# Kernel optimization log

Measured on AMD Instinct MI355X. Metric: run time of the kernel, lower is better.

## Reference

```python
import jax, jax.numpy as jnp
import numpy as np

BATCH, SEQ, D_MODEL = 8, 2048, 512
HEADS, BUCKET, N_HASHES = 8, 4, 4
D_HEAD = D_MODEL // HEADS
N_BUCKETS = SEQ // BUCKET
SELF_ATTN_VAL = -5e4  # TOKEN_SELF_ATTN_VALUE in reformer-pytorch


def setup_inputs() -> dict:
    key = jax.random.key(0)
    ks = jax.random.split(key, 8)
    scale = 1.0 / np.sqrt(D_MODEL).astype(np.float32)
    q = jax.random.normal(ks[0], (BATCH, SEQ, D_MODEL), jnp.float32)
    k = jax.random.normal(ks[1], (BATCH, SEQ, D_MODEL), jnp.float32)
    v = jax.random.normal(ks[2], (BATCH, SEQ, D_MODEL), jnp.float32)
    Wqk = jax.random.normal(ks[3], (D_MODEL, D_MODEL), jnp.float32) * scale
    Wv = jax.random.normal(ks[4], (D_MODEL, D_MODEL), jnp.float32) * scale
    Wout = jax.random.normal(ks[5], (D_MODEL, D_MODEL), jnp.float32) * scale
    b_out = jnp.zeros((D_MODEL,), jnp.float32)
    rotations = jax.random.normal(ks[6], (D_HEAD, N_HASHES, N_BUCKETS // 2), jnp.float32)
    return {"queries": q, "keys": k, "values": v, "Wqk": Wqk, "Wv": Wv,
            "Wout": Wout, "b_out": b_out, "rotations": rotations}


def _look_one_back(x):
    # concat each chunk with the previous chunk (wrap-around), along within-chunk axis
    return jnp.concatenate([x, jnp.roll(x, 1, axis=1)], axis=2)


def _lsh_attend(qk, v, rotations, bucket_size, n_hashes):
    # qk, v: (bm, t, d); shared-QK LSH attention (reformer-pytorch defaults)
    bm, t, d = qk.shape
    n_buckets = t // bucket_size
    # --- hash ---
    rotated = jnp.einsum('btf,fhi->bhti', qk, rotations)          # (bm, nh, t, nb/2)
    rotated = jnp.concatenate([rotated, -rotated], axis=-1)       # (bm, nh, t, nb)
    buckets = jnp.argmax(rotated, axis=-1)                        # (bm, nh, t)
    offsets = (jnp.arange(n_hashes) * n_buckets)[None, :, None]
    buckets = (buckets + offsets).reshape(bm, n_hashes * t)
    # --- sort tokens by (bucket, position) ---
    ticker = jnp.arange(n_hashes * t)
    buckets_and_t = t * buckets + (ticker % t)[None, :]           # unique values
    sticker = jnp.argsort(buckets_and_t, axis=-1)                 # (bm, nh*t)
    undo_sort = jnp.argsort(sticker, axis=-1)
    st = sticker % t
    sqk = jnp.take_along_axis(qk, st[:, :, None], axis=1)         # (bm, nh*t, d)
    sv = jnp.take_along_axis(v, st[:, :, None], axis=1)
    # --- chunk ---
    n_chunks = n_hashes * n_buckets
    bq_t = st.reshape(bm, n_chunks, bucket_size)
    bqk = sqk.reshape(bm, n_chunks, bucket_size, d)
    bv = sv.reshape(bm, n_chunks, bucket_size, d)
    bq = bqk
    norm = jnp.maximum(jnp.linalg.norm(bqk, axis=-1, keepdims=True), 1e-12)
    bk = bqk / norm                                               # F.normalize (shared QK)
    bk = _look_one_back(bk)
    bv = _look_one_back(bv)
    bkv_t = jnp.concatenate([bq_t, jnp.roll(bq_t, 1, axis=1)], axis=2)
    # --- attend within chunks ---
    dots = jnp.einsum('bnie,bnje->bnij', bq, bk) * (d ** -0.5)    # (bm, nc, bs, 2bs)
    self_mask = bq_t[:, :, :, None] == bkv_t[:, :, None, :]
    dots = jnp.where(self_mask, SELF_ATTN_VAL, dots)
    dots_lse = jax.nn.logsumexp(dots, axis=-1, keepdims=True)
    probs = jnp.exp(dots - dots_lse)
    bo = jnp.einsum('bnij,bnje->bnie', probs, bv)
    so = bo.reshape(bm, -1, d)
    slogits = dots_lse.reshape(bm, -1)
    # --- unsort and combine hash rounds ---
    o = jnp.take_along_axis(so, undo_sort[:, :, None], axis=1)
    logits = jnp.take_along_axis(slogits, undo_sort, axis=1)
    o = o.reshape(bm, n_hashes, t, d)
    logits = logits.reshape(bm, n_hashes, t, 1)
    w = jnp.exp(logits - jax.nn.logsumexp(logits, axis=1, keepdims=True))
    return jnp.sum(o * w, axis=1)                                 # (bm, t, d)


def reference(queries, keys, values, Wqk, Wv, Wout, b_out, rotations):
    # keys/values are unused by the original module (self-attention on queries)
    B, N, C = queries.shape
    H, d = HEADS, C // HEADS
    qk = jnp.einsum('bnc,cd->bnd', queries, Wqk)
    v = jnp.einsum('bnc,cd->bnd', queries, Wv)
    qk = qk.reshape(B, N, H, d).transpose(0, 2, 1, 3).reshape(B * H, N, d)
    v = v.reshape(B, N, H, d).transpose(0, 2, 1, 3).reshape(B * H, N, d)
    o = _lsh_attend(qk, v, rotations, BUCKET, N_HASHES)
    o = o.reshape(B, H, N, d).transpose(0, 2, 1, 3).reshape(B, N, C)
    return jnp.einsum('bnc,cd->bnd', o, Wout) + b_out
```

## Files before the change

kernel.cpp:

```cpp
#include <hip/hip_runtime.h>
#include <math.h>

#define SELF_VAL (-5e4f)

typedef __attribute__((ext_vector_type(8))) short bf16x8;
typedef __attribute__((ext_vector_type(4))) float f32x4;

__device__ __forceinline__ unsigned short f2bf(float x) {
    unsigned b = __float_as_uint(x);
    b += 0x7FFFu + ((b >> 16) & 1u);
    return (unsigned short)(b >> 16);
}
__device__ __forceinline__ float bf2f(unsigned short h) {
    return __uint_as_float(((unsigned)h) << 16);
}

__global__ __launch_bounds__(256) void k_rotT(const float* __restrict__ rot,
                                              float* __restrict__ rotT2)
{
    int idx = blockIdx.x * 256 + threadIdx.x;
    int h = idx >> 14, k = (idx >> 8) & 63, col = idx & 255;
    rotT2[idx] = rot[k * 1024 + h * 256 + col];
}

__global__ __launch_bounds__(256) void k_woutT(const float* __restrict__ Wout,
                                               unsigned short* __restrict__ WoutT16)
{
    int idx = blockIdx.x * 256 + threadIdx.x;
    int n = idx >> 9, k = idx & 511;
    WoutT16[idx] = f2bf(Wout[(size_t)k * 512 + n]);
}

__global__ __launch_bounds__(256) void k_wvT(const float* __restrict__ Wv,
                                             unsigned short* __restrict__ WvT16)
{
    int idx = blockIdx.x * 256 + threadIdx.x;
    int n = idx >> 9, k = idx & 511;
    WvT16[idx] = f2bf(Wv[(size_t)k * 512 + n]);
}

__global__ __launch_bounds__(256) void k_q16(const float* __restrict__ Q,
                                             unsigned short* __restrict__ Q16)
{
    int idx = blockIdx.x * 256 + threadIdx.x;
    const float* src = Q + (size_t)idx * 8;
    float4 v0 = *(const float4*)src;
    float4 v1 = *(const float4*)(src + 4);
    union { unsigned short s[8]; uint4 v; } ob;
    ob.s[0]=f2bf(v0.x); ob.s[1]=f2bf(v0.y); ob.s[2]=f2bf(v0.z); ob.s[3]=f2bf(v0.w);
    ob.s[4]=f2bf(v1.x); ob.s[5]=f2bf(v1.y); ob.s[6]=f2bf(v1.z); ob.s[7]=f2bf(v1.w);
    *(uint4*)(Q16 + (size_t)idx * 8) = ob.v;
}

__global__ __launch_bounds__(256) void k_gemm_qk(
    const float* __restrict__ Q, const float* __restrict__ Wqk,
    float* __restrict__ qk, float* __restrict__ rnorm)
{
    __shared__ float As[16][132];
    __shared__ float Bs[16][132];
    const int bx = blockIdx.x;
    const int mt = bx >> 2, nt = bx & 3;
    const int m0 = mt * 128, n0 = nt * 128;
    const int tid = threadIdx.x;
    const int ty = tid >> 4, tx = tid & 15;
    const float* Bsrc = Wqk + n0;
    const int ar0 = tid >> 2, acq = (tid & 3) * 4;
    const int ar1 = 64 + (tid >> 2);
    const int bk0 = tid >> 5, bnq = (tid & 31) * 4;
    const int bk1 = 8 + (tid >> 5);
    const float* Aptr0 = Q + (size_t)(m0 + ar0) * 512 + acq;
    const float* Aptr1 = Q + (size_t)(m0 + ar1) * 512 + acq;
    const float* Bptr0 = Bsrc + (size_t)bk0 * 512 + bnq;
    const float* Bptr1 = Bsrc + (size_t)bk1 * 512 + bnq;
    float acc[8][8] = {};
    float4 a0 = *(const float4*)(Aptr0);
    float4 a1 = *(const float4*)(Aptr1);
    float4 b0 = *(const float4*)(Bptr0);
    float4 b1 = *(const float4*)(Bptr1);
    for (int k0 = 0; k0 < 512; k0 += 16) {
        As[acq+0][ar0]=a0.x; As[acq+1][ar0]=a0.y; As[acq+2][ar0]=a0.z; As[acq+3][ar0]=a0.w;
        As[acq+0][ar1]=a1.x; As[acq+1][ar1]=a1.y; As[acq+2][ar1]=a1.z; As[acq+3][ar1]=a1.w;
        *(float4*)&Bs[bk0][bnq] = b0;
        *(float4*)&Bs[bk1][bnq] = b1;
        __syncthreads();
        if (k0 + 16 < 512) {
            a0 = *(const float4*)(Aptr0 + k0 + 16);
            a1 = *(const float4*)(Aptr1 + k0 + 16);
            b0 = *(const float4*)(Bptr0 + (size_t)(k0 + 16) * 512);
            b1 = *(const float4*)(Bptr1 + (size_t)(k0 + 16) * 512);
        }
        #pragma unroll
        for (int kk = 0; kk < 16; kk++) {
            float a_[8], b_[8];
            *(float4*)&a_[0] = *(float4*)&As[kk][ty*4];
            *(float4*)&a_[4] = *(float4*)&As[kk][64 + ty*4];
            *(float4*)&b_[0] = *(float4*)&Bs[kk][tx*4];
            *(float4*)&b_[4] = *(float4*)&Bs[kk][64 + tx*4];
            #pragma unroll
            for (int i = 0; i < 8; i++)
                #pragma unroll
                for (int j = 0; j < 8; j++)
                    acc[i][j] += a_[i] * b_[j];
        }
        __syncthreads();
    }
    #pragma unroll
    for (int ig = 0; ig < 2; ig++) {
        #pragma unroll
        for (int i = 0; i < 4; i++) {
            int row = m0 + ig*64 + ty*4 + i;
            int b = row >> 11, t = row & 2047;
            #pragma unroll
            for (int jg = 0; jg < 2; jg++) {
                int n = n0 + jg*64 + tx*4;
                float4 r4 = make_float4(acc[ig*4+i][jg*4+0], acc[ig*4+i][jg*4+1],
                                        acc[ig*4+i][jg*4+2], acc[ig*4+i][jg*4+3]);
                *(float4*)(qk + ((size_t)((b*8 + (n>>6))*2048 + t))*64 + (n&63)) = r4;
            }
        }
    }
    #pragma unroll
    for (int jg = 0; jg < 2; jg++) {
        int h = (n0 + jg*64) >> 6;
        #pragma unroll
        for (int ig = 0; ig < 2; ig++) {
            #pragma unroll
            for (int i = 0; i < 4; i++) {
                float s = acc[ig*4+i][jg*4+0]*acc[ig*4+i][jg*4+0]
                        + acc[ig*4+i][jg*4+1]*acc[ig*4+i][jg*4+1]
                        + acc[ig*4+i][jg*4+2]*acc[ig*4+i][jg*4+2]
                        + acc[ig*4+i][jg*4+3]*acc[ig*4+i][jg*4+3];
                s += __shfl_xor(s, 1);
                s += __shfl_xor(s, 2);
                s += __shfl_xor(s, 4);
                s += __shfl_xor(s, 8);
                if (tx == 0) {
                    int row = m0 + ig*64 + ty*4 + i;
                    int b = row >> 11, t = row & 2047;
                    rnorm[((size_t)(b*8 + h))*2048 + t] = 1.0f / fmaxf(sqrtf(s), 1e-12f);
                }
            }
        }
    }
}

__global__ __launch_bounds__(256) void k_gemm_v(
    const unsigned short* __restrict__ Q16, const unsigned short* __restrict__ WvT16,
    float* __restrict__ vv)
{
    __shared__ unsigned short Asl[64*72];
    __shared__ unsigned short Bsl[64*72];
    const int bx = blockIdx.x;
    const int mt = bx >> 3, nt = bx & 7;
    const int m0 = mt*64, n0 = nt*64;
    const int tid = threadIdx.x;
    const int wid = tid >> 6, lane = tid & 63;
    const int wm = wid >> 1, wn = wid & 1;
    const int l15 = lane & 15, l4 = lane >> 4;
    const int srow = tid >> 2, skb = (tid & 3) * 16;
    f32x4 acc[2][2] = {};
    for (int k0 = 0; k0 < 512; k0 += 64) {
        {
            const unsigned short* asrc = Q16 + (size_t)(m0 + srow)*512 + k0 + skb;
            *(uint4*)&Asl[srow*72 + skb]     = *(const uint4*)asrc;
            *(uint4*)&Asl[srow*72 + skb + 8] = *(const uint4*)(asrc + 8);
            const unsigned short* bsrc = WvT16 + (size_t)(n0 + srow)*512 + k0 + skb;
            *(uint4*)&Bsl[srow*72 + skb]     = *(const uint4*)bsrc;
            *(uint4*)&Bsl[srow*72 + skb + 8] = *(const uint4*)(bsrc + 8);
        }
        __syncthreads();
        #pragma unroll
        for (int kq = 0; kq < 2; kq++) {
            int kb = kq*32 + l4*8;
            bf16x8 a0 = *(bf16x8*)&Asl[(wm*32 +      l15)*72 + kb];
            bf16x8 a1 = *(bf16x8*)&Asl[(wm*32 + 16 + l15)*72 + kb];
            bf16x8 b0 = *(bf16x8*)&Bsl[(wn*32 +      l15)*72 + kb];
            bf16x8 b1 = *(bf16x8*)&Bsl[(wn*32 + 16 + l15)*72 + kb];
            acc[0][0] = __builtin_amdgcn_mfma_f32_16x16x32_bf16(a0, b0, acc[0][0], 0, 0, 0);
            acc[0][1] = __builtin_amdgcn_mfma_f32_16x16x32_bf16(a0, b1, acc[0][1], 0, 0, 0);
            acc[1][0] = __builtin_amdgcn_mfma_f32_16x16x32_bf16(a1, b0, acc[1][0], 0, 0, 0);
            acc[1][1] = __builtin_amdgcn_mfma_f32_16x16x32_bf16(a1, b1, acc[1][1], 0, 0, 0);
        }
        __syncthreads();
    }
    #pragma unroll
    for (int sm = 0; sm < 2; sm++) {
        #pragma unroll
        for (int sn = 0; sn < 2; sn++) {
            int col = n0 + wn*32 + sn*16 + l15;
            int h = col >> 6, d = col & 63;
            #pragma unroll
            for (int r = 0; r < 4; r++) {
                int row = m0 + wm*32 + sm*16 + l4*4 + r;
                int b = row >> 11, t = row & 2047;
                vv[((size_t)((b*8 + h)*2048 + t))*64 + d] = acc[sm][sn][r];
            }
        }
    }
}

__global__ __launch_bounds__(256) void k_hash(const float* __restrict__ qk,
    const float* __restrict__ rotT2, unsigned* __restrict__ buckets)
{
    __shared__ float As[64*128];
    const int bx = blockIdx.x;
    const int bm = bx >> 4;
    const int row0 = (bx & 15) << 7;
    const int tid = threadIdx.x;
    const int ty = tid >> 4, tx = tid & 15;
    {
        const int r = tid >> 1;
        const int kb = (tid & 1) * 8;
        const float* src = qk + ((size_t)(bm*2048 + row0 + r))*64;
        #pragma unroll
        for (int c = 0; c < 8; c++) {
            float4 a4 = *(const float4*)(src + (size_t)(kb + c)*4);
            int k = (kb + c)*4;
            As[(k+0)*128 + r] = a4.x;
            As[(k+1)*128 + r] = a4.y;
            As[(k+2)*128 + r] = a4.z;
            As[(k+3)*128 + r] = a4.w;
        }
    }
    __syncthreads();
    #pragma unroll 1
    for (int h = 0; h < 4; h++) {
        float bv[8]; unsigned bi[8];
        #pragma unroll
        for (int i = 0; i < 8; i++) { bv[i] = -3.402823466e38f; bi[i] = 0u; }
        #pragma unroll 1
        for (int ch = 0; ch < 4; ch++) {
            const float* bsrc = rotT2 + (size_t)h*16384 + ch*64 + tx*4;
            float acc[8][4] = {};
            #pragma unroll 16
            for (int kk = 0; kk < 64; kk++) {
                float4 b4 = *(const float4*)(bsrc + (size_t)kk*256);
                float a_[8];
                *(float4*)&a_[0] = *(float4*)&As[kk*128 + ty*4];
                *(float4*)&a_[4] = *(float4*)&As[kk*128 + 64 + ty*4];
                float b_[4] = {b4.x, b4.y, b4.z, b4.w};
                #pragma unroll
                for (int i = 0; i < 8; i++)
                    #pragma unroll
                    for (int j = 0; j < 4; j++)
                        acc[i][j] += a_[i] * b_[j];
            }
            #pragma unroll
            for (int j = 0; j < 4; j++) {
                unsigned c0 = (unsigned)(ch*64 + tx*4 + j);
                unsigned nc0 = 256u + c0;
                #pragma unroll
                for (int i = 0; i < 8; i++) {
                    float v = acc[i][j];
                    if (v > bv[i] || (v == bv[i] && c0 < bi[i])) { bv[i] = v; bi[i] = c0; }
                    float nv = -v;
                    if (nv > bv[i] || (nv == bv[i] && nc0 < bi[i])) { bv[i] = nv; bi[i] = nc0; }
                }
            }
        }
        #pragma unroll
        for (int i = 0; i < 8; i++) {
            #pragma unroll
            for (int d = 1; d < 16; d <<= 1) {
                float ov = __shfl_xor(bv[i], d);
                unsigned oi = (unsigned)__shfl_xor((int)bi[i], d);
                if (ov > bv[i] || (ov == bv[i] && oi < bi[i])) { bv[i] = ov; bi[i] = oi; }
            }
        }
        if (tx == 0) {
            #pragma unroll
            for (int i = 0; i < 8; i++) {
                int r = (i < 4) ? (ty*4 + i) : (64 + ty*4 + (i - 4));
                buckets[((size_t)(bm*4 + h))*2048 + row0 + r] = bi[i];
            }
        }
    }
}

__global__ __launch_bounds__(256) void k_sort(const unsigned* __restrict__ buckets,
                                              unsigned* __restrict__ st)
{
    __shared__ unsigned whist[4][512];
    __shared__ unsigned baseb[512];
    const int seg = blockIdx.x;
    const unsigned* bk = buckets + (size_t)seg * 2048;
    unsigned* out = st + (size_t)seg * 2048;
    const int tid = threadIdx.x, w = tid >> 6, lane = tid & 63;
    for (int b = tid; b < 2048; b += 256) ((unsigned*)whist)[b] = 0u;
    __syncthreads();
    unsigned myb[8];
    #pragma unroll
    for (int r = 0; r < 8; r++) {
        int pos = w*512 + r*64 + lane;
        myb[r] = bk[pos];
        atomicAdd(&whist[w][myb[r]], 1u);
    }
    __syncthreads();
    for (int b = tid; b < 512; b += 256) {
        unsigned p = 0;
        #pragma unroll
        for (int ww = 0; ww < 4; ww++) { unsigned t = whist[ww][b]; whist[ww][b] = p; p += t; }
        baseb[b] = p;
    }
    __syncthreads();
    if (tid == 0) {
        unsigned run = 0;
        for (int b = 0; b < 512; b++) { unsigned t = baseb[b]; baseb[b] = run; run += t; }
    }
    __syncthreads();
    for (int b = tid; b < 512; b += 256) {
        unsigned bb = baseb[b];
        #pragma unroll
        for (int ww = 0; ww < 4; ww++) whist[ww][b] += bb;
    }
    __syncthreads();
    for (int r = 0; r < 8; r++) {
        unsigned b = myb[r];
        int pos = w*512 + r*64 + lane;
        unsigned base = whist[w][b];
        unsigned rank = 0;
        for (int j = 0; j < 64; j++) {
            unsigned bj = __shfl(b, j);
            rank += (j < lane && bj == b) ? 1u : 0u;
        }
        out[base + rank] = (unsigned)pos;
        atomicAdd(&whist[w][b], 1u);
    }
}

__global__ __launch_bounds__(256) void k_attn(const float* __restrict__ qk,
    const float* __restrict__ vv, const float* __restrict__ rnorm,
    const unsigned* __restrict__ st, unsigned short* __restrict__ oh16,
    float* __restrict__ logits)
{
    __shared__ float qs[68][68];
    __shared__ float vs[68][68];
    __shared__ unsigned P[68];
    __shared__ float rn[68];
    const int sid = blockIdx.x;
    const int stripi = sid & 31;
    const int seg = sid >> 5;
    const int bm = seg >> 2, h = seg & 3;
    const int G0 = (h*512 + stripi*16) * 4;
    const int tid = threadIdx.x;
    for (int j = tid; j < 68; j += 256) {
        int G = (G0 - 4 + j) & 8191;
        int hg = G >> 11, sg = G & 2047;
        unsigned tok = st[((size_t)(bm*4 + hg))*2048 + sg];
        P[j] = tok;
        rn[j] = rnorm[bm*2048 + (int)tok];
    }
    __syncthreads();
    for (int e = tid; e < 68*16; e += 256) {
        int j = e >> 4, fq = e & 15;
        unsigned tok = P[j];
        size_t base = ((size_t)(bm*2048 + (int)tok))*64 + fq*4;
        *(float4*)&qs[j][fq*4] = *(const float4*)(qk + base);
        *(float4*)&vs[j][fq*4] = *(const float4*)(vv + base);
    }
    __syncthreads();
    const int w = tid >> 6, lane = tid & 63;
    const int half = lane >> 5, qi = (lane >> 3) & 3, jj = lane & 7;
    const int fb = lane & 7;
    for (int cp = 0; cp < 2; cp++) {
        int c = w*4 + cp*2 + half;
        int jq = 4 + c*4 + qi;
        int jk = c*4 + jj;
        float dot = 0.f;
        #pragma unroll
        for (int fq = 0; fq < 16; fq++) {
            float4 q4 = *(float4*)&qs[jq][fq*4];
            float4 k4 = *(float4*)&qs[jk][fq*4];
            dot += q4.x*k4.x + q4.y*k4.y + q4.z*k4.z + q4.w*k4.w;
        }
        dot *= 0.125f * rn[jk];
        if (P[jq] == P[jk]) dot = SELF_VAL;
        float m = dot;
        m = fmaxf(m, __shfl_xor(m, 1));
        m = fmaxf(m, __shfl_xor(m, 2));
        m = fmaxf(m, __shfl_xor(m, 4));
        float ex = expf(dot - m);
        float s = ex;
        s += __shfl_xor(s, 1); s += __shfl_xor(s, 2); s += __shfl_xor(s, 4);
        float lse = m + logf(s);
        float p = expf(dot - lse);
        unsigned tq = P[jq];
        if (jj == 0) logits[((size_t)(bm*4 + h))*2048 + tq] = lse;
        float a0=0,a1=0,a2=0,a3=0,a4a=0,a5=0,a6=0,a7=0;
        #pragma unroll
        for (int j2 = 0; j2 < 8; j2++) {
            float pj = __shfl(p, (lane & 0x38) | j2);
            float4 va = *(float4*)&vs[c*4 + j2][fb*8];
            float4 vb = *(float4*)&vs[c*4 + j2][fb*8 + 4];
            a0 += pj*va.x; a1 += pj*va.y; a2 += pj*va.z; a3 += pj*va.w;
            a4a += pj*vb.x; a5 += pj*vb.y; a6 += pj*vb.z; a7 += pj*vb.w;
        }
        union { unsigned short s[8]; uint4 v; } ob;
        ob.s[0]=f2bf(a0); ob.s[1]=f2bf(a1); ob.s[2]=f2bf(a2); ob.s[3]=f2bf(a3);
        ob.s[4]=f2bf(a4a); ob.s[5]=f2bf(a5); ob.s[6]=f2bf(a6); ob.s[7]=f2bf(a7);
        *(uint4*)(oh16 + ((size_t)((bm*4 + h)*2048 + (int)tq))*64 + fb*8) = ob.v;
    }
}

__global__ __launch_bounds__(256) void k_combine(const unsigned short* __restrict__ oh16,
    const float* __restrict__ logits, unsigned short* __restrict__ comb16)
{
    int w = threadIdx.x >> 6, lane = threadIdx.x & 63;
    int row = blockIdx.x * 4 + w;
    int bm = row >> 11, t = row & 2047;
    int b = bm >> 3, head = bm & 7;
    float l0 = logits[((size_t)(bm*4 + 0))*2048 + t];
    float l1 = logits[((size_t)(bm*4 + 1))*2048 + t];
    float l2 = logits[((size_t)(bm*4 + 2))*2048 + t];
    float l3 = logits[((size_t)(bm*4 + 3))*2048 + t];
    float m = fmaxf(fmaxf(l0, l1), fmaxf(l2, l3));
    float e0 = expf(l0 - m), e1 = expf(l1 - m), e2 = expf(l2 - m), e3 = expf(l3 - m);
    float inv = 1.0f / (e0 + e1 + e2 + e3);
    float o = 0.f;
    o += (e0*inv) * bf2f(oh16[((size_t)((bm*4+0)*2048 + t))*64 + lane]);
    o += (e1*inv) * bf2f(oh16[((size_t)((bm*4+1)*2048 + t))*64 + lane]);
    o += (e2*inv) * bf2f(oh16[((size_t)((bm*4+2)*2048 + t))*64 + lane]);
    o += (e3*inv) * bf2f(oh16[((size_t)((bm*4+3)*2048 + t))*64 + lane]);
    comb16[((size_t)(b*2048 + t))*512 + head*64 + lane] = f2bf(o);
}

__global__ __launch_bounds__(256) void k_gemm_out(
    const unsigned short* __restrict__ comb16, const unsigned short* __restrict__ WoutT16,
    const float* __restrict__ bias, float* __restrict__ out)
{
    __shared__ unsigned short Asl[64*72];
    __shared__ unsigned short Bsl[64*72];
    const int bx = blockIdx.x;
    const int mt = bx >> 3, nt = bx & 7;
    const int m0 = mt*64, n0 = nt*64;
    const int tid = threadIdx.x;
    const int wid = tid >> 6, lane = tid & 63;
    const int wm = wid >> 1, wn = wid & 1;
    const int l15 = lane & 15, l4 = lane >> 4;
    const int srow = tid >> 2, skb = (tid & 3) * 16;
    f32x4 acc[2][2] = {};
    for (int k0 = 0; k0 < 512; k0 += 64) {
        {
            const unsigned short* asrc = comb16 + (size_t)(m0 + srow)*512 + k0 + skb;
            *(uint4*)&Asl[srow*72 + skb]     = *(const uint4*)asrc;
            *(uint4*)&Asl[srow*72 + skb + 8] = *(const uint4*)(asrc + 8);
            const unsigned short* bsrc = WoutT16 + (size_t)(n0 + srow)*512 + k0 + skb;
            *(uint4*)&Bsl[srow*72 + skb]     = *(const uint4*)bsrc;
            *(uint4*)&Bsl[srow*72 + skb + 8] = *(const uint4*)(bsrc + 8);
        }
        __syncthreads();
        #pragma unroll
        for (int kq = 0; kq < 2; kq++) {
            int kb = kq*32 + l4*8;
            bf16x8 a0 = *(bf16x8*)&Asl[(wm*32 +      l15)*72 + kb];
            bf16x8 a1 = *(bf16x8*)&Asl[(wm*32 + 16 + l15)*72 + kb];
            bf16x8 b0 = *(bf16x8*)&Bsl[(wn*32 +      l15)*72 + kb];
            bf16x8 b1 = *(bf16x8*)&Bsl[(wn*32 + 16 + l15)*72 + kb];
            acc[0][0] = __builtin_amdgcn_mfma_f32_16x16x32_bf16(a0, b0, acc[0][0], 0, 0, 0);
            acc[0][1] = __builtin_amdgcn_mfma_f32_16x16x32_bf16(a0, b1, acc[0][1], 0, 0, 0);
            acc[1][0] = __builtin_amdgcn_mfma_f32_16x16x32_bf16(a1, b0, acc[1][0], 0, 0, 0);
            acc[1][1] = __builtin_amdgcn_mfma_f32_16x16x32_bf16(a1, b1, acc[1][1], 0, 0, 0);
        }
        __syncthreads();
    }
    #pragma unroll
    for (int sm = 0; sm < 2; sm++) {
        #pragma unroll
        for (int sn = 0; sn < 2; sn++) {
            int col = n0 + wn*32 + sn*16 + l15;
            float bb = bias[col];
            #pragma unroll
            for (int r = 0; r < 4; r++) {
                int row = m0 + wm*32 + sm*16 + l4*4 + r;
                out[(size_t)row*512 + col] = acc[sm][sn][r] + bb;
            }
        }
    }
}

extern "C" void kernel_launch(void* const* d_in, const int* in_sizes, int n_in,
                              void* d_out, int out_size, void* d_ws, size_t ws_size,
                              hipStream_t stream)
{
    const float* Q    = (const float*)d_in[0];
    const float* Wqk  = (const float*)d_in[3];
    const float* Wv   = (const float*)d_in[4];
    const float* Wout = (const float*)d_in[5];
    const float* bout = (const float*)d_in[6];
    const float* rot  = (const float*)d_in[7];
    float* ws = (float*)d_ws;
    float* qk     = ws;
    float* vv     = ws + 8388608;
    unsigned short* oh16 = (unsigned short*)(ws + 16777216);
    unsigned short* WoutT16 = (unsigned short*)(ws + 33554432);
    unsigned short* Q16     = (unsigned short*)(ws + 33685504);
    unsigned short* WvT16   = (unsigned short*)(ws + 37879808);
    unsigned short* comb16  = (unsigned short*)(ws + 50331648);
    float* rnorm  = ws + 58720256;
    float* logits = ws + 58851328;
    unsigned* buckets = (unsigned*)(ws + 59375616);
    unsigned* st      = (unsigned*)(ws + 59899904);
    float* rotT2  = ws + 60424192;
    float* out = (float*)d_out;

    k_rotT    <<<dim3(256),  dim3(256), 0, stream>>>(rot, rotT2);
    k_woutT   <<<dim3(1024), dim3(256), 0, stream>>>(Wout, WoutT16);
    k_wvT     <<<dim3(1024), dim3(256), 0, stream>>>(Wv, WvT16);
    k_q16     <<<dim3(4096), dim3(256), 0, stream>>>(Q, Q16);
    k_gemm_qk <<<dim3(512),  dim3(256), 0, stream>>>(Q, Wqk, qk, rnorm);
    k_gemm_v  <<<dim3(2048), dim3(256), 0, stream>>>(Q16, WvT16, vv);
    k_hash    <<<dim3(1024), dim3(256), 0, stream>>>(qk, rotT2, buckets);
    k_sort    <<<dim3(256),  dim3(256), 0, stream>>>(buckets, st);
    k_attn    <<<dim3(8192), dim3(256), 0, stream>>>(qk, vv, rnorm, st, oh16, logits);
    k_combine <<<dim3(32768),dim3(256), 0, stream>>>(oh16, logits, comb16);
    k_gemm_out<<<dim3(2048), dim3(256), 0, stream>>>(comb16, WoutT16, bout, out);
}
```

Measured before the change: 556.6 us.

## Compute LSH hash projections with split-bf16 MFMA and fp32 fallback near ties

The hash kernel's fp32 FMA projection is replaced by MFMA bf16 matrix ops. Operands are split into hi/lo bf16 parts (three products) to approximate fp32 precision. The kernel tracks the top-two scores per row, and rows whose gap falls below a threshold are recomputed exactly in fp32 so argmax ties still resolve like the reference. In exchange, the QK GEMM epilogue writes extra hi/lo buffers, a new rotation-split kernel is added, and the fallback path runs serialized block reductions.

```diff
diff --git a/kernel.cpp b/kernel.cpp
--- a/kernel.cpp
+++ b/kernel.cpp
@@ -2,6 +2,7 @@
 #include <math.h>
 
 #define SELF_VAL (-5e4f)
+#define GAP_THR 0.004f
 
 typedef __attribute__((ext_vector_type(8))) short bf16x8;
 typedef __attribute__((ext_vector_type(4))) float f32x4;
@@ -14,6 +15,9 @@
 __device__ __forceinline__ float bf2f(unsigned short h) {
     return __uint_as_float(((unsigned)h) << 16);
 }
+__device__ __forceinline__ unsigned pk2(unsigned short a, unsigned short b) {
+    return (unsigned)a | ((unsigned)b << 16);
+}
 
 __global__ __launch_bounds__(256) void k_rotT(const float* __restrict__ rot,
                                               float* __restrict__ rotT2)
@@ -21,6 +25,18 @@
     int idx = blockIdx.x * 256 + threadIdx.x;
     int h = idx >> 14, k = (idx >> 8) & 63, col = idx & 255;
     rotT2[idx] = rot[k * 1024 + h * 256 + col];
+}
+
+__global__ __launch_bounds__(256) void k_rotsplit(const float* __restrict__ rot,
+    unsigned short* __restrict__ rotT3hi, unsigned short* __restrict__ rotT3lo)
+{
+    int idx = blockIdx.x * 256 + threadIdx.x;
+    int cg = idx >> 6, k = idx & 63;
+    float v = rot[k * 1024 + cg];
+    unsigned short hi = f2bf(v);
+    unsigned short lo = f2bf(v - bf2f(hi));
+    rotT3hi[idx] = hi;
+    rotT3lo[idx] = lo;
 }
 
 __global__ __launch_bounds__(256) void k_woutT(const float* __restrict__ Wout,
@@ -54,7 +70,8 @@
 
 __global__ __launch_bounds__(256) void k_gemm_qk(
     const float* __restrict__ Q, const float* __restrict__ Wqk,
-    float* __restrict__ qk, float* __restrict__ rnorm)
+    float* __restrict__ qk, float* __restrict__ rnorm,
+    unsigned short* __restrict__ qk16hi, unsigned short* __restrict__ qk16lo)
 {
     __shared__ float As[16][132];
     __shared__ float Bs[16][132];
@@ -115,7 +132,15 @@
                 int n = n0 + jg*64 + tx*4;
                 float4 r4 = make_float4(acc[ig*4+i][jg*4+0], acc[ig*4+i][jg*4+1],
                                         acc[ig*4+i][jg*4+2], acc[ig*4+i][jg*4+3]);
-                *(float4*)(qk + ((size_t)((b*8 + (n>>6))*2048 + t))*64 + (n&63)) = r4;
+                size_t base = ((size_t)((b*8 + (n>>6))*2048 + t))*64 + (n&63);
+                *(float4*)(qk + base) = r4;
+                unsigned short h0 = f2bf(r4.x), h1 = f2bf(r4.y), h2 = f2bf(r4.z), h3 = f2bf(r4.w);
+                unsigned short l0 = f2bf(r4.x - bf2f(h0)), l1 = f2bf(r4.y - bf2f(h1));
+                unsigned short l2 = f2bf(r4.z - bf2f(h2)), l3 = f2bf(r4.w - bf2f(h3));
+                uint2 hw = make_uint2(pk2(h0,h1), pk2(h2,h3));
+                uint2 lw = make_uint2(pk2(l0,l1), pk2(l2,l3));
+                *(uint2*)(qk16hi + base) = hw;
+                *(uint2*)(qk16lo + base) = lw;
             }
         }
     }
@@ -199,79 +224,157 @@
     }
 }
 
-__global__ __launch_bounds__(256) void k_hash(const float* __restrict__ qk,
-    const float* __restrict__ rotT2, unsigned* __restrict__ buckets)
-{
-    __shared__ float As[64*128];
-    const int bx = blockIdx.x;
-    const int bm = bx >> 4;
-    const int row0 = (bx & 15) << 7;
+__global__ __launch_bounds__(256) void k_hash(
+    const float* __restrict__ qk,
+    const unsigned short* __restrict__ qk16hi, const unsigned short* __restrict__ qk16lo,
+    const float* __restrict__ rotT2,
+    const unsigned short* __restrict__ rotT3hi, const unsigned short* __restrict__ rotT3lo,
+    unsigned* __restrict__ buckets)
+{
+    __shared__ unsigned short Ahi[64*72], Alo[64*72], Bhi[64*72], Blo[64*72];
+    __shared__ float redv1[128], redv2[128];
+    __shared__ unsigned redi1[128];
+    __shared__ float fv[256];
+    __shared__ unsigned fi[256];
+    __shared__ unsigned bidx[64];
+    __shared__ int bflag[64];
+    const int m0 = blockIdx.x * 64;
     const int tid = threadIdx.x;
-    const int ty = tid >> 4, tx = tid & 15;
+    const int wid = tid >> 6, lane = tid & 63;
+    const int wm = wid >> 1, wn = wid & 1;
+    const int l15 = lane & 15, l4 = lane >> 4;
+    const int srow = tid >> 2, skb = (tid & 3) * 16;
     {
-        const int r = tid >> 1;
-        const int kb = (tid & 1) * 8;
-        const float* src = qk + ((size_t)(bm*2048 + row0 + r))*64;
-        #pragma unroll
-        for (int c = 0; c < 8; c++) {
-            float4 a4 = *(const float4*)(src + (size_t)(kb + c)*4);
-            int k = (kb + c)*4;
-            As[(k+0)*128 + r] = a4.x;
-            As[(k+1)*128 + r] = a4.y;
-            As[(k+2)*128 + r] = a4.z;
-            As[(k+3)*128 + r] = a4.w;
-        }
-    }
-    __syncthreads();
-    #pragma unroll 1
-    for (int h = 0; h < 4; h++) {
-        float bv[8]; unsigned bi[8];
-        #pragma unroll
-        for (int i = 0; i < 8; i++) { bv[i] = -3.402823466e38f; bi[i] = 0u; }
-        #pragma unroll 1
-        for (int ch = 0; ch < 4; ch++) {
-            const float* bsrc = rotT2 + (size_t)h*16384 + ch*64 + tx*4;
-            float acc[8][4] = {};
-            #pragma unroll 16
-            for (int kk = 0; kk < 64; kk++) {
-                float4 b4 = *(const float4*)(bsrc + (size_t)kk*256);
-                float a_[8];
-                *(float4*)&a_[0] = *(float4*)&As[kk*128 + ty*4];
-                *(float4*)&a_[4] = *(float4*)&As[kk*128 + 64 + ty*4];
-                float b_[4] = {b4.x, b4.y, b4.z, b4.w};
+        const unsigned short* ah = qk16hi + (size_t)(m0 + srow)*64 + skb;
+        const unsigned short* al = qk16lo + (size_t)(m0 + srow)*64 + skb;
+        *(uint4*)&Ahi[srow*72 + skb]     = *(const uint4*)ah;
+        *(uint4*)&Ahi[srow*72 + skb + 8] = *(const uint4*)(ah + 8);
+        *(uint4*)&Alo[srow*72 + skb]     = *(const uint4*)al;
+        *(uint4*)&Alo[srow*72 + skb + 8] = *(const uint4*)(al + 8);
+    }
+    float bv1[8], bv2[8];
+    unsigned bi1[8];
+    for (int ch = 0; ch < 16; ch++) {
+        const int h = ch >> 2;
+        if ((ch & 3) == 0) {
+            #pragma unroll
+            for (int i = 0; i < 8; i++) { bv1[i] = -3.402823466e38f; bv2[i] = -3.402823466e38f; bi1[i] = 0u; }
+        }
+        __syncthreads();
+        {
+            const unsigned short* bh = rotT3hi + (size_t)(ch*64 + srow)*64 + skb;
+            const unsigned short* bl = rotT3lo + (size_t)(ch*64 + srow)*64 + skb;
+            *(uint4*)&Bhi[srow*72 + skb]     = *(const uint4*)bh;
+            *(uint4*)&Bhi[srow*72 + skb + 8] = *(const uint4*)(bh + 8);
+            *(uint4*)&Blo[srow*72 + skb]     = *(const uint4*)bl;
+            *(uint4*)&Blo[srow*72 + skb + 8] = *(const uint4*)(bl + 8);
+        }
+        __syncthreads();
+        f32x4 acc[2][2] = {};
+        #pragma unroll
+        for (int kq = 0; kq < 2; kq++) {
+            int kb = kq*32 + l4*8;
+            bf16x8 ah0 = *(bf16x8*)&Ahi[(wm*32 +      l15)*72 + kb];
+            bf16x8 ah1 = *(bf16x8*)&Ahi[(wm*32 + 16 + l15)*72 + kb];
+            bf16x8 al0 = *(bf16x8*)&Alo[(wm*32 +      l15)*72 + kb];
+            bf16x8 al1 = *(bf16x8*)&Alo[(wm*32 + 16 + l15)*72 + kb];
+            bf16x8 bh0 = *(bf16x8*)&Bhi[(wn*32 +      l15)*72 + kb];
+            bf16x8 bh1 = *(bf16x8*)&Bhi[(wn*32 + 16 + l15)*72 + kb];
+            bf16x8 bl0 = *(bf16x8*)&Blo[(wn*32 +      l15)*72 + kb];
+            bf16x8 bl1 = *(bf16x8*)&Blo[(wn*32 + 16 + l15)*72 + kb];
+            acc[0][0] = __builtin_amdgcn_mfma_f32_16x16x32_bf16(ah0, bh0, acc[0][0], 0, 0, 0);
+            acc[0][1] = __builtin_amdgcn_mfma_f32_16x16x32_bf16(ah0, bh1, acc[0][1], 0, 0, 0);
+            acc[1][0] = __builtin_amdgcn_mfma_f32_16x16x32_bf16(ah1, bh0, acc[1][0], 0, 0, 0);
+            acc[1][1] = __builtin_amdgcn_mfma_f32_16x16x32_bf16(ah1, bh1, acc[1][1], 0, 0, 0);
+            acc[0][0] = __builtin_amdgcn_mfma_f32_16x16x32_bf16(ah0, bl0, acc[0][0], 0, 0, 0);
+            acc[0][1] = __builtin_amdgcn_mfma_f32_16x16x32_bf16(ah0, bl1, acc[0][1], 0, 0, 0);
+            acc[1][0] = __builtin_amdgcn_mfma_f32_16x16x32_bf16(ah1, bl0, acc[1][0], 0, 0, 0);
+            acc[1][1] = __builtin_amdgcn_mfma_f32_16x16x32_bf16(ah1, bl1, acc[1][1], 0, 0, 0);
+            acc[0][0] = __builtin_amdgcn_mfma_f32_16x16x32_bf16(al0, bh0, acc[0][0], 0, 0, 0);
+            acc[0][1] = __builtin_amdgcn_mfma_f32_16x16x32_bf16(al0, bh1, acc[0][1], 0, 0, 0);
+            acc[1][0] = __builtin_amdgcn_mfma_f32_16x16x32_bf16(al1, bh0, acc[1][0], 0, 0, 0);
+            acc[1][1] = __builtin_amdgcn_mfma_f32_16x16x32_bf16(al1, bh1, acc[1][1], 0, 0, 0);
+        }
+        #pragma unroll
+        for (int sm = 0; sm < 2; sm++) {
+            #pragma unroll
+            for (int sn = 0; sn < 2; sn++) {
+                unsigned ci = (unsigned)((ch & 3)*64 + wn*32 + sn*16 + l15);
                 #pragma unroll
-                for (int i = 0; i < 8; i++)
-                    #pragma unroll
-                    for (int j = 0; j < 4; j++)
-                        acc[i][j] += a_[i] * b_[j];
-            }
-            #pragma unroll
-            for (int j = 0; j < 4; j++) {
-                unsigned c0 = (unsigned)(ch*64 + tx*4 + j);
-                unsigned nc0 = 256u + c0;
+                for (int r = 0; r < 4; r++) {
+                    int ri = sm*4 + r;
+                    float v = acc[sm][sn][r];
+                    if (v > bv1[ri]) { bv2[ri] = bv1[ri]; bv1[ri] = v; bi1[ri] = ci; }
+                    else if (v > bv2[ri]) bv2[ri] = v;
+                    float nv = -v;
+                    if (nv > bv1[ri]) { bv2[ri] = bv1[ri]; bv1[ri] = nv; bi1[ri] = 256u + ci; }
+                    else if (nv > bv2[ri]) bv2[ri] = nv;
+                }
+            }
+        }
+        if ((ch & 3) == 3) {
+            #pragma unroll
+            for (int i = 0; i < 8; i++) {
+                #pragma unroll
+                for (int d = 1; d < 16; d <<= 1) {
+                    float ov1 = __shfl_xor(bv1[i], d);
+                    unsigned oi1 = (unsigned)__shfl_xor((int)bi1[i], d);
+                    float ov2 = __shfl_xor(bv2[i], d);
+                    if (ov1 > bv1[i]) { bv2[i] = fmaxf(bv1[i], ov2); bv1[i] = ov1; bi1[i] = oi1; }
+                    else if (ov1 < bv1[i]) { bv2[i] = fmaxf(bv2[i], ov1); }
+                    else { bi1[i] = min(bi1[i], oi1); bv2[i] = bv1[i]; }
+                }
+            }
+            if (l15 == 0) {
                 #pragma unroll
                 for (int i = 0; i < 8; i++) {
-                    float v = acc[i][j];
-                    if (v > bv[i] || (v == bv[i] && c0 < bi[i])) { bv[i] = v; bi[i] = c0; }
-                    float nv = -v;
-                    if (nv > bv[i] || (nv == bv[i] && nc0 < bi[i])) { bv[i] = nv; bi[i] = nc0; }
+                    int rl = wm*32 + (i >> 2)*16 + l4*4 + (i & 3);
+                    redv1[wn*64 + rl] = bv1[i];
+                    redi1[wn*64 + rl] = bi1[i];
+                    redv2[wn*64 + rl] = bv2[i];
                 }
             }
-        }
-        #pragma unroll
-        for (int i = 0; i < 8; i++) {
-            #pragma unroll
-            for (int d = 1; d < 16; d <<= 1) {
-                float ov = __shfl_xor(bv[i], d);
-                unsigned oi = (unsigned)__shfl_xor((int)bi[i], d);
-                if (ov > bv[i] || (ov == bv[i] && oi < bi[i])) { bv[i] = ov; bi[i] = oi; }
-            }
-        }
-        if (tx == 0) {
-            #pragma unroll
-            for (int i = 0; i < 8; i++) {
-                int r = (i < 4) ? (ty*4 + i) : (64 + ty*4 + (i - 4));
-                buckets[((size_t)(bm*4 + h))*2048 + row0 + r] = bi[i];
+            __syncthreads();
+            if (tid < 64) {
+                float v1 = redv1[tid], v2 = redv2[tid];
+                unsigned i1 = redi1[tid];
+                float w1 = redv1[64 + tid], w2 = redv2[64 + tid];
+                unsigned j1 = redi1[64 + tid];
+                float nv1, nv2; unsigned ni1;
+                if (w1 > v1)      { nv1 = w1; ni1 = j1; nv2 = fmaxf(v1, w2); }
+                else if (w1 < v1) { nv1 = v1; ni1 = i1; nv2 = fmaxf(v2, w1); }
+                else              { nv1 = v1; ni1 = min(i1, j1); nv2 = v1; }
+                bidx[tid] = ni1;
+                bflag[tid] = (nv1 - nv2 < GAP_THR) ? 1 : 0;
+            }
+            __syncthreads();
+            for (int r = 0; r < 64; r++) {
+                if (bflag[r]) {
+                    const float* qrow = qk + (size_t)(m0 + r) * 64;
+                    const float* rc = rotT2 + (size_t)h * 16384 + tid;
+                    float dsum = 0.f;
+                    #pragma unroll 16
+                    for (int k = 0; k < 64; k++) dsum += qrow[k] * rc[k * 256];
+                    float mv; unsigned mi;
+                    if (dsum >= -dsum) { mv = dsum; mi = (unsigned)tid; }
+                    else               { mv = -dsum; mi = 256u + (unsigned)tid; }
+                    fv[tid] = mv; fi[tid] = mi;
+                    __syncthreads();
+                    for (int s = 128; s > 0; s >>= 1) {
+                        if (tid < s) {
+                            float ov = fv[tid + s]; unsigned oi = fi[tid + s];
+                            if (ov > fv[tid] || (ov == fv[tid] && oi < fi[tid])) { fv[tid] = ov; fi[tid] = oi; }
+                        }
+                        __syncthreads();
+                    }
+                    if (tid == 0) bidx[r] = fi[0];
+                    __syncthreads();
+                }
+            }
+            if (tid < 64) {
+                int grow = m0 + tid;
+                int bm = grow >> 11, t = grow & 2047;
+                buckets[((size_t)(bm*4 + h))*2048 + t] = bidx[tid];
             }
         }
     }
@@ -491,10 +594,14 @@
     float* ws = (float*)d_ws;
     float* qk     = ws;
     float* vv     = ws + 8388608;
-    unsigned short* oh16 = (unsigned short*)(ws + 16777216);
+    unsigned short* oh16    = (unsigned short*)(ws + 16777216);
     unsigned short* WoutT16 = (unsigned short*)(ws + 33554432);
     unsigned short* Q16     = (unsigned short*)(ws + 33685504);
     unsigned short* WvT16   = (unsigned short*)(ws + 37879808);
+    unsigned short* qk16hi  = (unsigned short*)(ws + 38010880);
+    unsigned short* qk16lo  = (unsigned short*)(ws + 42205184);
+    unsigned short* rotT3hi = (unsigned short*)(ws + 46399488);
+    unsigned short* rotT3lo = (unsigned short*)(ws + 46432256);
     unsigned short* comb16  = (unsigned short*)(ws + 50331648);
     float* rnorm  = ws + 58720256;
     float* logits = ws + 58851328;
@@ -504,12 +611,13 @@
     float* out = (float*)d_out;
 
     k_rotT    <<<dim3(256),  dim3(256), 0, stream>>>(rot, rotT2);
+    k_rotsplit<<<dim3(256),  dim3(256), 0, stream>>>(rot, rotT3hi, rotT3lo);
     k_woutT   <<<dim3(1024), dim3(256), 0, stream>>>(Wout, WoutT16);
     k_wvT     <<<dim3(1024), dim3(256), 0, stream>>>(Wv, WvT16);
     k_q16     <<<dim3(4096), dim3(256), 0, stream>>>(Q, Q16);
-    k_gemm_qk <<<dim3(512),  dim3(256), 0, stream>>>(Q, Wqk, qk, rnorm);
+    k_gemm_qk <<<dim3(512),  dim3(256), 0, stream>>>(Q, Wqk, qk, rnorm, qk16hi, qk16lo);
     k_gemm_v  <<<dim3(2048), dim3(256), 0, stream>>>(Q16, WvT16, vv);
-    k_hash    <<<dim3(1024), dim3(256), 0, stream>>>(qk, rotT2, buckets);
+    k_hash    <<<dim3(2048), dim3(256), 0, stream>>>(qk, qk16hi, qk16lo, rotT2, rotT3hi, rotT3lo, buckets);
     k_sort    <<<dim3(256),  dim3(256), 0, stream>>>(buckets, st);
     k_attn    <<<dim3(8192), dim3(256), 0, stream>>>(qk, vv, rnorm, st, oh16, logits);
     k_combine <<<dim3(32768),dim3(256), 0, stream>>>(oh16, logits, comb16);
```

After: 605.2 us. 1.09x slower.
